# Kernel optimization log

Measured on AMD Instinct MI355X. Metric: run time of the kernel, lower is better.

## Reference

```python
import jax, jax.numpy as jnp
import numpy as np


def setup_inputs() -> dict:
    key = jax.random.key(0)
    ks = jax.random.split(key, 10)
    B, T = 1024, 8192
    # X features: [time, current I, temperature T, voltage U]
    t = jnp.cumsum(jax.random.uniform(ks[0], (B, T, 1), jnp.float32) + 0.5, axis=1)  # increasing time
    feats = jax.random.normal(ks[1], (B, T, 3), jnp.float32)
    X = jnp.concatenate([t, feats], axis=-1)  # [B, T, 4]
    # SC: [Q (capacity), eta_0, R, SOC_init_base]; keep Q away from 0
    SC = jax.random.uniform(ks[2], (B, 4), jnp.float32, minval=0.5, maxval=1.5)
    std = 0.1
    # SOC_init_net: Linear(4,1) -> Softplus -> Linear(1,1), normal(0,0.1) weights, zero bias
    W1i = jax.random.normal(ks[3], (1, 4), jnp.float32) * std
    b1i = jnp.zeros((1,), jnp.float32)
    W2i = jax.random.normal(ks[4], (1, 1), jnp.float32) * std
    b2i = jnp.zeros((1,), jnp.float32)
    # eta_net: Linear(2,1) -> Softplus -> Linear(1,1)
    W1e = jax.random.normal(ks[5], (1, 2), jnp.float32) * std
    b1e = jnp.zeros((1,), jnp.float32)
    W2e = jax.random.normal(ks[6], (1, 1), jnp.float32) * std
    b2e = jnp.zeros((1,), jnp.float32)
    return {"X": X, "SC": SC, "W1i": W1i, "b1i": b1i, "W2i": W2i, "b2i": b2i,
            "W1e": W1e, "b1e": b1e, "W2e": W2e, "b2e": b2e}


def reference(X, SC, W1i, b1i, W2i, b2i, W1e, b1e, W2e, b2e):
    # X: [B, T, 4] = (t, I, Temp, U); SC: [B, 4] = (Q, eta_0, R, soc_base)
    I = X[..., 1:2]      # [B, T, 1]
    Temp = X[..., 2:3]   # [B, T, 1]
    U = X[..., 3:4]      # [B, T, 1]
    R = SC[..., 2:3]     # [B, 1]
    # SOC_init_net on first-timestep features
    feat0 = jnp.concatenate([I[:, 0, :], Temp[:, 0, :], U[:, 0, :], R], axis=-1)  # [B, 4]
    h0 = jax.nn.softplus(feat0 @ W1i.T + b1i)
    soc_net = h0 @ W2i.T + b2i                     # [B, 1]
    SOC_init = SC[..., 3:4] * (1.0 + soc_net)      # [B, 1]
    # eta_net over all timesteps
    feat = jnp.concatenate([I, Temp], axis=-1)     # [B, T, 2]
    h = jax.nn.softplus(feat @ W1e.T + b1e)
    delta_eta = h @ W2e.T + b2e                    # [B, T, 1]
    # ODE RHS: dSOC/dt = eta_0 * (1 + delta_eta) * I / (3600 * Q)
    Q = SC[..., 0:1][:, None, :]                   # [B, 1, 1]
    eta0 = SC[..., 1:2][:, None, :]                # [B, 1, 1]
    f = eta0 * (1.0 + delta_eta) * I / (3600.0 * Q)  # [B, T, 1]
    # Euler integration: y_{k+1} = y_k + (t_{k+1} - t_k) * f(x_k, y_k); f independent of y -> cumsum
    ts = X[..., 0:1]                               # [B, T, 1]
    dt = ts[:, 1:] - ts[:, :-1]                    # [B, T-1, 1]
    incr = dt * f[:, :-1]                          # [B, T-1, 1]
    zero = jnp.zeros_like(SOC_init)[:, None, :]    # [B, 1, 1]
    SOC = SOC_init[:, None, :] + jnp.concatenate([zero, jnp.cumsum(incr, axis=1)], axis=1)
    return SOC                                     # [B, T, 1]
```

## Files before the change

### kernel.cpp

```cpp
#include <hip/hip_runtime.h>
#include <type_traits>


static __device__ __forceinline__ float bf2f(unsigned int u) {
    union { unsigned int i; float f; } v;
    v.i = u << 16;
    return v.f;
}
static __device__ __forceinline__ unsigned short f2bf(float f) {
    union { unsigned int i; float f; } v;
    v.f = f;
    unsigned int x = v.i;
    return (unsigned short)((x + 0x7fffu + ((x >> 16) & 1u)) >> 16);
}
static __device__ __forceinline__ float sp_fast(float x) {
    return __logf(1.f + __expf(x));
}

struct F4 { float ts, I, Te, U; };
static __device__ __forceinline__ F4 dec(ushort4 x) {
    return {bf2f(x.x), bf2f(x.y), bf2f(x.z), bf2f(x.w)};
}
static __device__ __forceinline__ F4 dec(float4 x) {
    return {x.x, x.y, x.z, x.w};
}

template <bool BF16>
static __device__ __forceinline__ float ld(const void* p, int i) {
    return BF16 ? bf2f(((const unsigned short*)p)[i]) : ((const float*)p)[i];
}

constexpr int BLOCK = 256;

__global__ __launch_bounds__(BLOCK, 6) void socnet_tot(
    const void* __restrict__ Xv, const void* __restrict__ SCv,
    const void* __restrict__ W1iv, const void* __restrict__ b1iv,
    const void* __restrict__ W2iv, const void* __restrict__ b2iv,
    const void* __restrict__ W1ev, const void* __restrict__ b1ev,
    const void* __restrict__ W2ev, const void* __restrict__ b2ev,
    float* __restrict__ ws, int B)
{
    const float* X   = (const float*)Xv;
    const float* SC  = (const float*)SCv;
    const float* W1i = (const float*)W1iv;
    const float* b1i = (const float*)b1iv;
    const float* W2i = (const float*)W2iv;
    const float* b2i = (const float*)b2iv;
    const float* W1e = (const float*)W1ev;
    const float* b1e = (const float*)b1ev;
    const float* W2e = (const float*)W2ev;
    const float* b2e = (const float*)b2ev;

    const int blk  = blockIdx.x;
    const int b    = blk >> 3;
    const int s    = blk & 7;
    const int tid  = threadIdx.x;
    const int lane = tid & 63;
    const int wave = tid >> 6;

    const float Q    = SC[b * 4 + 0];
    const float eta0 = SC[b * 4 + 1];
    const float Rsc  = SC[b * 4 + 2];
    const float S3   = SC[b * 4 + 3];
    const float w1e0 = W1e[0];
    const float w1e1 = W1e[1];
    const float vb1e = b1e[0];
    const float coef = eta0 / (3600.f * Q);
    const float c2   = coef * W2e[0];
    const float c1   = coef * (1.f + b2e[0]);

    const float4* Xrow = (const float4*)X + (size_t)b * 8192;
    const int base = s * 1024;

    const float4 v0 = Xrow[base + tid * 4 + 0];
    const float4 v1 = Xrow[base + tid * 4 + 1];
    const float4 v2 = Xrow[base + tid * 4 + 2];
    const float4 v3 = Xrow[base + tid * 4 + 3];

    float4 vp; float ts_c, f_c;
    if (s == 0 && wave == 0) {
        vp = Xrow[0];
        ts_c = vp.x;
        f_c  = 0.f;
    } else {
        vp = Xrow[base + wave * 256 - 1];
        ts_c = vp.x;
        f_c  = fmaf(c2, sp_fast(fmaf(vp.y, w1e0, fmaf(vp.z, w1e1, vb1e))), c1) * vp.y;
    }

    const float f0 = fmaf(c2, sp_fast(fmaf(v0.y, w1e0, fmaf(v0.z, w1e1, vb1e))), c1) * v0.y;
    const float f1 = fmaf(c2, sp_fast(fmaf(v1.y, w1e0, fmaf(v1.z, w1e1, vb1e))), c1) * v1.y;
    const float f2 = fmaf(c2, sp_fast(fmaf(v2.y, w1e0, fmaf(v2.z, w1e1, vb1e))), c1) * v2.y;
    const float f3 = fmaf(c2, sp_fast(fmaf(v3.y, w1e0, fmaf(v3.z, w1e1, vb1e))), c1) * v3.y;

    float pts = __shfl_up(v3.x, 1, 64);
    float pf  = __shfl_up(f3,   1, 64);
    if (lane == 0) { pts = ts_c; pf = f_c; }

    float gsum = (v0.x - pts) * pf;
    gsum = fmaf(v1.x - v0.x, f0, gsum);
    gsum = fmaf(v2.x - v1.x, f1, gsum);
    gsum = fmaf(v3.x - v2.x, f2, gsum);

    #pragma unroll
    for (int d = 1; d < 64; d <<= 1)
        gsum += __shfl_xor(gsum, d, 64);

    __shared__ float sred[4];
    if (lane == 0) sred[wave] = gsum;
    __syncthreads();
    if (tid == 0)
        ws[b * 8 + s] = sred[0] + sred[1] + sred[2] + sred[3];

    if (s == 0 && tid == 0) {
        const float pre = fmaf(vp.y, W1i[0],
                          fmaf(vp.z, W1i[1],
                          fmaf(vp.w, W1i[2],
                          fmaf(Rsc, W1i[3], b1i[0]))));
        ws[B * 8 + b] = S3 * (1.f + fmaf(sp_fast(pre), W2i[0], b2i[0]));
    }
}

__global__ __launch_bounds__(BLOCK, 6) void socnet_scan(
    const void* __restrict__ Xv, const void* __restrict__ SCv,
    const void* __restrict__ W1ev, const void* __restrict__ b1ev,
    const void* __restrict__ W2ev, const void* __restrict__ b2ev,
    const float* __restrict__ ws, void* __restrict__ outv, int B)
{
    const float* X   = (const float*)Xv;
    const float* SC  = (const float*)SCv;
    const float* W1e = (const float*)W1ev;
    const float* b1e = (const float*)b1ev;
    const float* W2e = (const float*)W2ev;
    const float* b2e = (const float*)b2ev;

    const int blk  = blockIdx.x;
    const int b    = blk >> 3;
    const int s    = blk & 7;
    const int tid  = threadIdx.x;
    const int lane = tid & 63;
    const int wave = tid >> 6;

    const float Q    = SC[b * 4 + 0];
    const float eta0 = SC[b * 4 + 1];
    const float w1e0 = W1e[0];
    const float w1e1 = W1e[1];
    const float vb1e = b1e[0];
    const float coef = eta0 / (3600.f * Q);
    const float c2   = coef * W2e[0];
    const float c1   = coef * (1.f + b2e[0]);

    float bacc = ws[B * 8 + b];
    #pragma unroll
    for (int j = 0; j < 7; ++j)
        if (j < s) bacc += ws[b * 8 + j];

    const float4* Xrow = (const float4*)X + (size_t)b * 8192;
    const int base = s * 1024;

    const float4 v0 = Xrow[base + tid * 4 + 0];
    const float4 v1 = Xrow[base + tid * 4 + 1];
    const float4 v2 = Xrow[base + tid * 4 + 2];
    const float4 v3 = Xrow[base + tid * 4 + 3];

    float4 vp; float ts_c, f_c;
    if (s == 0 && wave == 0) {
        vp = Xrow[0];
        ts_c = vp.x;
        f_c  = 0.f;
    } else {
        vp = Xrow[base + wave * 256 - 1];
        ts_c = vp.x;
        f_c  = fmaf(c2, sp_fast(fmaf(vp.y, w1e0, fmaf(vp.z, w1e1, vb1e))), c1) * vp.y;
    }

    const float f0 = fmaf(c2, sp_fast(fmaf(v0.y, w1e0, fmaf(v0.z, w1e1, vb1e))), c1) * v0.y;
    const float f1 = fmaf(c2, sp_fast(fmaf(v1.y, w1e0, fmaf(v1.z, w1e1, vb1e))), c1) * v1.y;
    const float f2 = fmaf(c2, sp_fast(fmaf(v2.y, w1e0, fmaf(v2.z, w1e1, vb1e))), c1) * v2.y;
    const float f3 = fmaf(c2, sp_fast(fmaf(v3.y, w1e0, fmaf(v3.z, w1e1, vb1e))), c1) * v3.y;

    float pts = __shfl_up(v3.x, 1, 64);
    float pf  = __shfl_up(f3,   1, 64);
    if (lane == 0) { pts = ts_c; pf = f_c; }

    const float g0 = (v0.x - pts) * pf;
    const float g1 = fmaf(v1.x - v0.x, f0, g0);
    const float g2 = fmaf(v2.x - v1.x, f1, g1);
    const float g3 = fmaf(v3.x - v2.x, f2, g2);

    float S = g3;
    #pragma unroll
    for (int d = 1; d < 64; d <<= 1) {
        const float u = __shfl_up(S, d, 64);
        if (lane >= d) S += u;
    }

    __shared__ float swt[4];
    if (lane == 63) swt[wave] = S;
    __syncthreads();

    float add = bacc + (S - g3);
    #pragma unroll
    for (int w = 0; w < 3; ++w)
        if (w < wave) add += swt[w];

    float4 o;
    o.x = g0 + add;
    o.y = g1 + add;
    o.z = g2 + add;
    o.w = g3 + add;
    ((float4*)outv)[(size_t)b * 2048 + s * 256 + tid] = o;
}

template <int NCH>
static __device__ void scan_k4(
    const float* __restrict__ X, const float* __restrict__ SC,
    const float* __restrict__ W1i, const float* __restrict__ b1i,
    const float* __restrict__ W2i, const float* __restrict__ b2i,
    const float* __restrict__ W1e, const float* __restrict__ b1e,
    const float* __restrict__ W2e, const float* __restrict__ b2e,
    float* __restrict__ outv, float* s_wtot, float* s_init)
{
    constexpr int SPAN = NCH * 256;
    constexpr int T    = SPAN * 4;

    const int b    = blockIdx.x;
    const int tid  = threadIdx.x;
    const int lane = tid & 63;
    const int wave = tid >> 6;
    const int ws   = wave * SPAN;

    const float Q    = SC[b * 4 + 0];
    const float eta0 = SC[b * 4 + 1];
    const float R    = SC[b * 4 + 2];
    const float S3   = SC[b * 4 + 3];
    const float w1e0 = W1e[0];
    const float w1e1 = W1e[1];
    const float vb1e = b1e[0];
    const float coef = eta0 / (3600.f * Q);
    const float c2   = coef * W2e[0];
    const float c1   = coef * (1.f + b2e[0]);

    const float4* Xrow = (const float4*)X + (size_t)b * T;

    float4 ring[8];
    #pragma unroll
    for (int c = 0; c < 2; ++c)
        #pragma unroll
        for (int j = 0; j < 4; ++j)
            ring[c * 4 + j] = Xrow[ws + c * 256 + lane * 4 + j];

    float ts_c, f_c;
    if (wave > 0) {
        const float4 vp = Xrow[ws - 1];
        const float hp = sp_fast(fmaf(vp.y, w1e0, fmaf(vp.z, w1e1, vb1e)));
        f_c  = fmaf(c2, hp, c1) * vp.y;
        ts_c = vp.x;
    } else {
        const float4 v0 = Xrow[0];
        ts_c = v0.x;
        f_c  = 0.f;
        const float pre = fmaf(v0.y, W1i[0],
                          fmaf(v0.z, W1i[1],
                          fmaf(v0.w, W1i[2],
                          fmaf(R, W1i[3], b1i[0]))));
        const float h0 = sp_fast(pre);
        if (lane == 0)
            *s_init = S3 * (1.f + fmaf(h0, W2i[0], b2i[0]));
    }

    float vals[NCH * 4];
    float carry = 0.f;
    #pragma unroll
    for (int c = 0; c < NCH; ++c) {
        const int s = (c & 1) * 4;
        const float4 v0 = ring[s + 0];
        const float4 v1 = ring[s + 1];
        const float4 v2 = ring[s + 2];
        const float4 v3 = ring[s + 3];
        if (c + 2 < NCH) {
            #pragma unroll
            for (int j = 0; j < 4; ++j)
                ring[s + j] = Xrow[ws + (c + 2) * 256 + lane * 4 + j];
        }

        const float f0 = fmaf(c2, sp_fast(fmaf(v0.y, w1e0, fmaf(v0.z, w1e1, vb1e))), c1) * v0.y;
        const float f1 = fmaf(c2, sp_fast(fmaf(v1.y, w1e0, fmaf(v1.z, w1e1, vb1e))), c1) * v1.y;
        const float f2 = fmaf(c2, sp_fast(fmaf(v2.y, w1e0, fmaf(v2.z, w1e1, vb1e))), c1) * v2.y;
        const float f3 = fmaf(c2, sp_fast(fmaf(v3.y, w1e0, fmaf(v3.z, w1e1, vb1e))), c1) * v3.y;

        float pts = __shfl_up(v3.x, 1, 64);
        float pf  = __shfl_up(f3,   1, 64);
        if (lane == 0) { pts = ts_c; pf = f_c; }

        const float g0 = (v0.x - pts) * pf;
        const float g1 = fmaf(v1.x - v0.x, f0, g0);
        const float g2 = fmaf(v2.x - v1.x, f1, g1);
        const float g3 = fmaf(v3.x - v2.x, f2, g2);

        float S = g3;
        #pragma unroll
        for (int d = 1; d < 64; d <<= 1) {
            const float u = __shfl_up(S, d, 64);
            if (lane >= d) S += u;
        }
        const float tb = carry + (S - g3);
        vals[c * 4 + 0] = g0 + tb;
        vals[c * 4 + 1] = g1 + tb;
        vals[c * 4 + 2] = g2 + tb;
        vals[c * 4 + 3] = g3 + tb;

        carry += __shfl(S, 63, 64);
        ts_c   = __shfl(v3.x, 63, 64);
        f_c    = __shfl(f3, 63, 64);
    }
    if (lane == 0) s_wtot[wave] = carry;
    __syncthreads();

    float base = *s_init;
    #pragma unroll
    for (int w = 0; w < 3; ++w)
        if (w < wave) base += s_wtot[w];

    float4* orow = (float4*)(outv + (size_t)b * T);
    #pragma unroll
    for (int c = 0; c < NCH; ++c) {
        float4 o;
        o.x = vals[c * 4 + 0] + base;
        o.y = vals[c * 4 + 1] + base;
        o.z = vals[c * 4 + 2] + base;
        o.w = vals[c * 4 + 3] + base;
        orow[wave * (SPAN / 4) + c * 64 + lane] = o;
    }
}

__global__ __launch_bounds__(BLOCK, 4) void socnet_reg(
    const void* __restrict__ X, const void* __restrict__ SC,
    const void* __restrict__ W1i, const void* __restrict__ b1i,
    const void* __restrict__ W2i, const void* __restrict__ b2i,
    const void* __restrict__ W1e, const void* __restrict__ b1e,
    const void* __restrict__ W2e, const void* __restrict__ b2e,
    void* __restrict__ out)
{
    __shared__ float s_wtot[4];
    __shared__ float s_init;
    scan_k4<8>((const float*)X, (const float*)SC,
               (const float*)W1i, (const float*)b1i,
               (const float*)W2i, (const float*)b2i,
               (const float*)W1e, (const float*)b1e,
               (const float*)W2e, (const float*)b2e,
               (float*)out, s_wtot, &s_init);
}

template <bool BF16>
static __device__ void scan_serial(
    const void* __restrict__ Xv, const void* __restrict__ SCv,
    const void* __restrict__ W1i, const void* __restrict__ b1i,
    const void* __restrict__ W2i, const void* __restrict__ b2i,
    const void* __restrict__ W1e, const void* __restrict__ b1e,
    const void* __restrict__ W2e, const void* __restrict__ b2e,
    void* __restrict__ outv, int T,
    float* s_wts, float* s_wf, float* s_wsum, float* s_carr)
{
    using XVec = typename std::conditional<BF16, ushort4, float4>::type;
    const int b = blockIdx.x, tid = threadIdx.x;
    const int lane = tid & 63, wave = tid >> 6;
    const int ntile = (T + BLOCK - 1) / BLOCK;

    const float Q    = ld<BF16>(SCv, b * 4 + 0);
    const float eta0 = ld<BF16>(SCv, b * 4 + 1);
    const float R    = ld<BF16>(SCv, b * 4 + 2);
    const float S3   = ld<BF16>(SCv, b * 4 + 3);
    const float w1e0 = ld<BF16>(W1e, 0);
    const float w1e1 = ld<BF16>(W1e, 1);
    const float vb1e = ld<BF16>(b1e, 0);
    const float coef = eta0 / (3600.f * Q);
    const float c2   = coef * ld<BF16>(W2e, 0);
    const float c1   = coef * (1.f + ld<BF16>(b2e, 0));

    const XVec* Xrow = (const XVec*)Xv + (size_t)b * T;

    for (int tile = 0; tile < ntile; ++tile) {
        const int t = tile * BLOCK + tid;
        const bool act = t < T;
        F4 v = {0.f, 0.f, 0.f, 0.f};
        if (act) v = dec(Xrow[t]);
        const float f = fmaf(c2, sp_fast(fmaf(v.I, w1e0, fmaf(v.Te, w1e1, vb1e))), c1) * v.I;

        float pts = __shfl_up(v.ts, 1, 64);
        float pf  = __shfl_up(f, 1, 64);

        __syncthreads();
        if (lane == 63) { s_wts[wave] = v.ts; s_wf[wave] = f; }
        if (tile == 0 && tid == 0) {
            const float pre = fmaf(v.I, ld<BF16>(W1i, 0),
                              fmaf(v.Te, ld<BF16>(W1i, 1),
                              fmaf(v.U, ld<BF16>(W1i, 2),
                              fmaf(R, ld<BF16>(W1i, 3), ld<BF16>(b1i, 0)))));
            s_carr[0] = S3 * (1.f + fmaf(sp_fast(pre), ld<BF16>(W2i, 0), ld<BF16>(b2i, 0)));
        }
        __syncthreads();
        if (lane == 0) {
            if (wave == 0) { if (tile > 0) { pts = s_carr[1]; pf = s_carr[2]; } }
            else { pts = s_wts[wave - 1]; pf = s_wf[wave - 1]; }
        }
        float g = (t == 0 || !act) ? 0.f : (v.ts - pts) * pf;
        #pragma unroll
        for (int d = 1; d < 64; d <<= 1) {
            const float u = __shfl_up(g, d, 64);
            if (lane >= d) g += u;
        }
        if (lane == 63) s_wsum[wave] = g;
        __syncthreads();
        float soc = s_carr[0];
        #pragma unroll
        for (int w = 0; w < 3; ++w) if (w < wave) soc += s_wsum[w];
        soc += g;
        if (act) {
            if (BF16) ((unsigned short*)outv)[(size_t)b * T + t] = f2bf(soc);
            else      ((float*)outv)[(size_t)b * T + t] = soc;
        }
        __syncthreads();
        if (tid == BLOCK - 1) { s_carr[0] = soc; s_carr[1] = v.ts; s_carr[2] = f; }
    }
}

__global__ __launch_bounds__(BLOCK) void socnet_serial_k(
    const void* __restrict__ X, const void* __restrict__ SC,
    const void* __restrict__ W1i, const void* __restrict__ b1i,
    const void* __restrict__ W2i, const void* __restrict__ b2i,
    const void* __restrict__ W1e, const void* __restrict__ b1e,
    const void* __restrict__ W2e, const void* __restrict__ b2e,
    void* __restrict__ out, int T)
{
    __shared__ float s_wts[4], s_wf[4], s_wsum[4], s_carr[3];
    const unsigned int* scw = (const unsigned int*)SC;
    const float l0 = bf2f(scw[0] & 0xFFFFu), l1 = bf2f(scw[1] & 0xFFFFu);
    const float l2 = bf2f(scw[2] & 0xFFFFu), l3 = bf2f(scw[3] & 0xFFFFu);
    const bool isbf =
        (l0 >= 0.45f && l0 <= 1.55f) && (l1 >= 0.45f && l1 <= 1.55f) &&
        (l2 >= 0.45f && l2 <= 1.55f) && (l3 >= 0.45f && l3 <= 1.55f);
    if (isbf) scan_serial<true >(X, SC, W1i, b1i, W2i, b2i, W1e, b1e, W2e, b2e,
                                 out, T, s_wts, s_wf, s_wsum, s_carr);
    else      scan_serial<false>(X, SC, W1i, b1i, W2i, b2i, W1e, b1e, W2e, b2e,
                                 out, T, s_wts, s_wf, s_wsum, s_carr);
}

extern "C" void kernel_launch(void* const* d_in, const int* in_sizes, int n_in,
                              void* d_out, int out_size, void* d_ws, size_t ws_size,
                              hipStream_t stream) {
    const int B = in_sizes[1] / 4;
    const int T = in_sizes[0] / (B * 4);

    const size_t ws_need = (size_t)(B * 9) * sizeof(float);

    if (T == 8192 && ws_size >= ws_need && d_ws != nullptr) {
        socnet_tot<<<dim3(B * 8), dim3(BLOCK), 0, stream>>>(
            d_in[0], d_in[1], d_in[2], d_in[3], d_in[4], d_in[5],
            d_in[6], d_in[7], d_in[8], d_in[9], (float*)d_ws, B);
        socnet_scan<<<dim3(B * 8), dim3(BLOCK), 0, stream>>>(
            d_in[0], d_in[1],
            d_in[6], d_in[7], d_in[8], d_in[9],
            (const float*)d_ws, d_out, B);
    } else if (T == 8192) {
        socnet_reg<<<dim3(B), dim3(BLOCK), 0, stream>>>(
            d_in[0], d_in[1], d_in[2], d_in[3], d_in[4], d_in[5],
            d_in[6], d_in[7], d_in[8], d_in[9], d_out);
    } else {
        socnet_serial_k<<<dim3(B), dim3(BLOCK), 0, stream>>>(
            d_in[0], d_in[1], d_in[2], d_in[3], d_in[4], d_in[5],
            d_in[6], d_in[7], d_in[8], d_in[9], d_out, T);
    }
}
```

Before: 231.7 us.

## Fuse reduce and scan passes into single-pass chained scan with flags

Merges the two-kernel reduce-then-scan into one kernel. Each block publishes its segment total through a flagged 64-bit word in workspace and waits on the flags of earlier segments in the same row to get its base offset. This removes the second full read of the input, which is the main memory cost. In exchange it adds a flag-zeroing launch, serial spin-waits on predecessors, and relies on blocks being scheduled in order to avoid deadlock.

```diff
diff --git a/kernel.cpp b/kernel.cpp
--- a/kernel.cpp
+++ b/kernel.cpp
@@ -32,13 +32,20 @@
 
 constexpr int BLOCK = 256;
 
-__global__ __launch_bounds__(BLOCK, 6) void socnet_tot(
+__global__ __launch_bounds__(BLOCK) void socnet_zero(
+    unsigned long long* __restrict__ w, int n)
+{
+    const int i = blockIdx.x * BLOCK + threadIdx.x;
+    if (i < n) w[i] = 0ULL;
+}
+
+__global__ __launch_bounds__(BLOCK, 8) void socnet_lb(
     const void* __restrict__ Xv, const void* __restrict__ SCv,
     const void* __restrict__ W1iv, const void* __restrict__ b1iv,
     const void* __restrict__ W2iv, const void* __restrict__ b2iv,
     const void* __restrict__ W1ev, const void* __restrict__ b1ev,
     const void* __restrict__ W2ev, const void* __restrict__ b2ev,
-    float* __restrict__ ws, int B)
+    unsigned long long* __restrict__ wsb, void* __restrict__ outv, int B)
 {
     const float* X   = (const float*)Xv;
     const float* SC  = (const float*)SCv;
@@ -60,8 +67,6 @@
 
     const float Q    = SC[b * 4 + 0];
     const float eta0 = SC[b * 4 + 1];
-    const float Rsc  = SC[b * 4 + 2];
-    const float S3   = SC[b * 4 + 3];
     const float w1e0 = W1e[0];
     const float w1e1 = W1e[1];
     const float vb1e = b1e[0];
@@ -97,92 +102,6 @@
     float pf  = __shfl_up(f3,   1, 64);
     if (lane == 0) { pts = ts_c; pf = f_c; }
 
-    float gsum = (v0.x - pts) * pf;
-    gsum = fmaf(v1.x - v0.x, f0, gsum);
-    gsum = fmaf(v2.x - v1.x, f1, gsum);
-    gsum = fmaf(v3.x - v2.x, f2, gsum);
-
-    #pragma unroll
-    for (int d = 1; d < 64; d <<= 1)
-        gsum += __shfl_xor(gsum, d, 64);
-
-    __shared__ float sred[4];
-    if (lane == 0) sred[wave] = gsum;
-    __syncthreads();
-    if (tid == 0)
-        ws[b * 8 + s] = sred[0] + sred[1] + sred[2] + sred[3];
-
-    if (s == 0 && tid == 0) {
-        const float pre = fmaf(vp.y, W1i[0],
-                          fmaf(vp.z, W1i[1],
-                          fmaf(vp.w, W1i[2],
-                          fmaf(Rsc, W1i[3], b1i[0]))));
-        ws[B * 8 + b] = S3 * (1.f + fmaf(sp_fast(pre), W2i[0], b2i[0]));
-    }
-}
-
-__global__ __launch_bounds__(BLOCK, 6) void socnet_scan(
-    const void* __restrict__ Xv, const void* __restrict__ SCv,
-    const void* __restrict__ W1ev, const void* __restrict__ b1ev,
-    const void* __restrict__ W2ev, const void* __restrict__ b2ev,
-    const float* __restrict__ ws, void* __restrict__ outv, int B)
-{
-    const float* X   = (const float*)Xv;
-    const float* SC  = (const float*)SCv;
-    const float* W1e = (const float*)W1ev;
-    const float* b1e = (const float*)b1ev;
-    const float* W2e = (const float*)W2ev;
-    const float* b2e = (const float*)b2ev;
-
-    const int blk  = blockIdx.x;
-    const int b    = blk >> 3;
-    const int s    = blk & 7;
-    const int tid  = threadIdx.x;
-    const int lane = tid & 63;
-    const int wave = tid >> 6;
-
-    const float Q    = SC[b * 4 + 0];
-    const float eta0 = SC[b * 4 + 1];
-    const float w1e0 = W1e[0];
-    const float w1e1 = W1e[1];
-    const float vb1e = b1e[0];
-    const float coef = eta0 / (3600.f * Q);
-    const float c2   = coef * W2e[0];
-    const float c1   = coef * (1.f + b2e[0]);
-
-    float bacc = ws[B * 8 + b];
-    #pragma unroll
-    for (int j = 0; j < 7; ++j)
-        if (j < s) bacc += ws[b * 8 + j];
-
-    const float4* Xrow = (const float4*)X + (size_t)b * 8192;
-    const int base = s * 1024;
-
-    const float4 v0 = Xrow[base + tid * 4 + 0];
-    const float4 v1 = Xrow[base + tid * 4 + 1];
-    const float4 v2 = Xrow[base + tid * 4 + 2];
-    const float4 v3 = Xrow[base + tid * 4 + 3];
-
-    float4 vp; float ts_c, f_c;
-    if (s == 0 && wave == 0) {
-        vp = Xrow[0];
-        ts_c = vp.x;
-        f_c  = 0.f;
-    } else {
-        vp = Xrow[base + wave * 256 - 1];
-        ts_c = vp.x;
-        f_c  = fmaf(c2, sp_fast(fmaf(vp.y, w1e0, fmaf(vp.z, w1e1, vb1e))), c1) * vp.y;
-    }
-
-    const float f0 = fmaf(c2, sp_fast(fmaf(v0.y, w1e0, fmaf(v0.z, w1e1, vb1e))), c1) * v0.y;
-    const float f1 = fmaf(c2, sp_fast(fmaf(v1.y, w1e0, fmaf(v1.z, w1e1, vb1e))), c1) * v1.y;
-    const float f2 = fmaf(c2, sp_fast(fmaf(v2.y, w1e0, fmaf(v2.z, w1e1, vb1e))), c1) * v2.y;
-    const float f3 = fmaf(c2, sp_fast(fmaf(v3.y, w1e0, fmaf(v3.z, w1e1, vb1e))), c1) * v3.y;
-
-    float pts = __shfl_up(v3.x, 1, 64);
-    float pf  = __shfl_up(f3,   1, 64);
-    if (lane == 0) { pts = ts_c; pf = f_c; }
-
     const float g0 = (v0.x - pts) * pf;
     const float g1 = fmaf(v1.x - v0.x, f0, g0);
     const float g2 = fmaf(v2.x - v1.x, f1, g1);
@@ -195,14 +114,42 @@
         if (lane >= d) S += u;
     }
 
-    __shared__ float swt[4];
-    if (lane == 63) swt[wave] = S;
+    __shared__ float s_wt[4];
+    __shared__ float s_base;
+    if (lane == 63) s_wt[wave] = S;
     __syncthreads();
 
-    float add = bacc + (S - g3);
+    if (tid == 0) {
+        const float seg_total = s_wt[0] + s_wt[1] + s_wt[2] + s_wt[3];
+        const unsigned long long pub =
+            (1ULL << 32) | (unsigned long long)__float_as_uint(seg_total);
+        __hip_atomic_store(&wsb[blk], pub, __ATOMIC_RELEASE,
+                           __HIP_MEMORY_SCOPE_AGENT);
+
+        const float4 x0 = Xrow[0];
+        const float pre = fmaf(x0.y, W1i[0],
+                          fmaf(x0.z, W1i[1],
+                          fmaf(x0.w, W1i[2],
+                          fmaf(SC[b * 4 + 2], W1i[3], b1i[0]))));
+        float bacc = SC[b * 4 + 3] *
+                     (1.f + fmaf(sp_fast(pre), W2i[0], b2i[0]));
+
+        for (int j = 0; j < s; ++j) {
+            unsigned long long v;
+            do {
+                v = __hip_atomic_load(&wsb[b * 8 + j], __ATOMIC_ACQUIRE,
+                                      __HIP_MEMORY_SCOPE_AGENT);
+            } while (!(v >> 32));
+            bacc += __uint_as_float((unsigned int)v);
+        }
+        s_base = bacc;
+    }
+    __syncthreads();
+
+    float add = s_base + (S - g3);
     #pragma unroll
     for (int w = 0; w < 3; ++w)
-        if (w < wave) add += swt[w];
+        if (w < wave) add += s_wt[w];
 
     float4 o;
     o.x = g0 + add;
@@ -452,16 +399,17 @@
     const int B = in_sizes[1] / 4;
     const int T = in_sizes[0] / (B * 4);
 
-    const size_t ws_need = (size_t)(B * 9) * sizeof(float);
+    const int    nflags  = B * 8;
+    const size_t ws_need = (size_t)nflags * sizeof(unsigned long long);
 
     if (T == 8192 && ws_size >= ws_need && d_ws != nullptr) {
-        socnet_tot<<<dim3(B * 8), dim3(BLOCK), 0, stream>>>(
+        const int zgrid = (nflags + BLOCK - 1) / BLOCK;
+        socnet_zero<<<dim3(zgrid), dim3(BLOCK), 0, stream>>>(
+            (unsigned long long*)d_ws, nflags);
+        socnet_lb<<<dim3(B * 8), dim3(BLOCK), 0, stream>>>(
             d_in[0], d_in[1], d_in[2], d_in[3], d_in[4], d_in[5],
-            d_in[6], d_in[7], d_in[8], d_in[9], (float*)d_ws, B);
-        socnet_scan<<<dim3(B * 8), dim3(BLOCK), 0, stream>>>(
-            d_in[0], d_in[1],
             d_in[6], d_in[7], d_in[8], d_in[9],
-            (const float*)d_ws, d_out, B);
+            (unsigned long long*)d_ws, d_out, B);
     } else if (T == 8192) {
         socnet_reg<<<dim3(B), dim3(BLOCK), 0, stream>>>(
             d_in[0], d_in[1], d_in[2], d_in[3], d_in[4], d_in[5],
```

Result: slower. 760.8 us (+228.4%).
